# Kernel tuning notes

Hardware: AMD Instinct MI355X
Metric: run time of the kernel (lower is better)

## Reference

```python
import jax, jax.numpy as jnp
import numpy as np


def insert_tdl(tdl, x):
    # Shift delay line: newest sample at row 0, drop oldest row.
    return jnp.concatenate([x, tdl[:-1]], axis=0)


def setup_inputs() -> dict:
    key = jax.random.key(0)
    ks = jax.random.split(key, 17)
    B = 16384            # batch of parallel simulations (columns)
    H = 1024             # controller hidden size
    Hp = 1024            # plant hidden size
    Dci = Dcr = Dco = 64 # controller TDL depths
    Dpi = Dpo = 64       # plant TDL depths
    f = lambda k, s: jax.random.normal(k, s, dtype=jnp.float32)
    return {
        "reference": f(ks[0], (1, B)),
        "citdl": f(ks[1], (Dci, B)),
        "crtdl": f(ks[2], (Dcr, B)),
        "cotdl": f(ks[3], (Dco, B)),
        "pitdl": f(ks[4], (Dpi - 1, B)),  # fresh controller output a2 completes the line
        "potdl": f(ks[5], (Dpo, B)),
        # controller parameters (trainable in the original)
        "ciw": 0.01 * f(ks[6], (H, Dci)),
        "crw": 0.01 * f(ks[7], (H, Dcr)),
        "cow": 0.01 * f(ks[8], (H, Dco)),
        "cb1": 0.01 * f(ks[9], (H, 1)),
        "clw": 0.01 * f(ks[10], (1, H)),
        "cb2": 0.01 * f(ks[11], (1, 1)),
        # plant parameters (detached/frozen in the original)
        "piw": 0.01 * f(ks[12], (Hp, Dpi)),
        "p_ow": 0.01 * f(ks[13], (Hp, Dpo)),
        "pb1": 0.01 * f(ks[14], (Hp, 1)),
        "plw": 0.01 * f(ks[15], (1, Hp)),
        "pb2": 0.01 * f(ks[16], (1, 1)),
    }


def reference(reference, citdl, crtdl, cotdl, pitdl, potdl,
              ciw, crw, cow, cb1, clw, cb2,
              piw, p_ow, pb1, plw, pb2):
    # Controller MLP
    n1 = ciw @ citdl + crw @ crtdl + cow @ cotdl + cb1   # [H, B]
    a1 = jnp.tanh(n1)
    a2 = clw @ a1 + cb2                                   # [1, B] controller output
    # Plant MLP (frozen model of the plant)
    pdelay = jnp.concatenate([pitdl, a2], axis=0)         # [Dpi, B]
    n3 = piw @ pdelay + p_ow @ potdl + pb1                # [Hp, B]
    a3 = jnp.tanh(n3)
    a4 = plw @ a3 + pb2                                   # [1, B] plant output
    # TDL shift/insert updates
    citdl = insert_tdl(citdl, a2)
    crtdl = insert_tdl(crtdl, reference)
    cotdl = insert_tdl(cotdl, a4)
    pitdl = insert_tdl(pitdl, a2)
    potdl = insert_tdl(potdl, a4)
    return (a4, citdl, crtdl, cotdl, pitdl, potdl)
```

## Files before the change

### kernel.cpp

```cpp
#include <hip/hip_runtime.h>

#define B_COLS 16384
#define BT 64
#define NWAVES 8
#define NT 4
#define X1_STRIDE 200
#define X2_STRIDE 136

#define OFS_A4 0
#define OFS_CI 16384
#define OFS_CR 1064960
#define OFS_CO 2113536
#define OFS_PI 3162112
#define OFS_PO 4194304

typedef short bf16x8_t __attribute__((ext_vector_type(8)));
typedef float f32x4_t __attribute__((ext_vector_type(4)));

__device__ __forceinline__ unsigned short bftrunc(float f) {
    return (unsigned short)(__float_as_uint(f) >> 16);
}
__device__ __forceinline__ unsigned int pk2(float lo, float hi) {
    return __builtin_amdgcn_perm(__float_as_uint(hi), __float_as_uint(lo), 0x07060302u);
}
__device__ __forceinline__ float tanh_fast(float x) {
    x = fminf(1.5f, fmaxf(-1.5f, x));
    float x2 = x * x;
    float num = x * (15.0f + x2);
    float den = 15.0f + 6.0f * x2;
    return num * __builtin_amdgcn_rcpf(den);
}

extern "C" __global__ __launch_bounds__(512, 2)
void fused_cell(const float* __restrict__ ref,
                const float* __restrict__ citdl,
                const float* __restrict__ crtdl,
                const float* __restrict__ cotdl,
                const float* __restrict__ pitdl,
                const float* __restrict__ potdl,
                const float* __restrict__ ciw,
                const float* __restrict__ crw,
                const float* __restrict__ cow,
                const float* __restrict__ cb1,
                const float* __restrict__ clw,
                const float* __restrict__ cb2,
                const float* __restrict__ piw,
                const float* __restrict__ p_ow,
                const float* __restrict__ pb1,
                const float* __restrict__ plw,
                const float* __restrict__ pb2,
                float* __restrict__ out)
{
    __shared__ unsigned short X1T[BT * X1_STRIDE];
    __shared__ unsigned short X2T[BT * X2_STRIDE];
    __shared__ float redbuf[NWAVES * BT];

    const int tid  = threadIdx.x;
    const int wave = tid >> 6;
    const int lane = tid & 63;
    const int quad = lane >> 4;
    const int l15  = lane & 15;
    const int c0   = blockIdx.x * BT;

    {
        const int w8 = wave * 8;
        #pragma unroll
        for (int pass = 0; pass < 3; ++pass) {
            int k = pass * 64 + lane;
            const float* src; int d;
            if (k < 64)       { src = citdl; d = k; }
            else if (k < 128) { src = crtdl; d = k - 64; }
            else              { src = cotdl; d = k - 128; }
            const float* p = src + (size_t)d * B_COLS + c0 + w8;
            float4 v0 = *(const float4*)(p);
            float4 v1 = *(const float4*)(p + 4);
            unsigned short* dst = &X1T[w8 * X1_STRIDE + k];
            dst[0 * X1_STRIDE] = bftrunc(v0.x);
            dst[1 * X1_STRIDE] = bftrunc(v0.y);
            dst[2 * X1_STRIDE] = bftrunc(v0.z);
            dst[3 * X1_STRIDE] = bftrunc(v0.w);
            dst[4 * X1_STRIDE] = bftrunc(v1.x);
            dst[5 * X1_STRIDE] = bftrunc(v1.y);
            dst[6 * X1_STRIDE] = bftrunc(v1.z);
            dst[7 * X1_STRIDE] = bftrunc(v1.w);
        }
        #pragma unroll
        for (int pass = 0; pass < 2; ++pass) {
            int k = pass * 64 + lane;
            if (k != 63) {
                const float* src; int d;
                if (k < 63) { src = pitdl; d = k; }
                else        { src = potdl; d = k - 64; }
                const float* p = src + (size_t)d * B_COLS + c0 + w8;
                float4 v0 = *(const float4*)(p);
                float4 v1 = *(const float4*)(p + 4);
                unsigned short* dst = &X2T[w8 * X2_STRIDE + k];
                dst[0 * X2_STRIDE] = bftrunc(v0.x);
                dst[1 * X2_STRIDE] = bftrunc(v0.y);
                dst[2 * X2_STRIDE] = bftrunc(v0.z);
                dst[3 * X2_STRIDE] = bftrunc(v0.w);
                dst[4 * X2_STRIDE] = bftrunc(v1.x);
                dst[5 * X2_STRIDE] = bftrunc(v1.y);
                dst[6 * X2_STRIDE] = bftrunc(v1.z);
                dst[7 * X2_STRIDE] = bftrunc(v1.w);
            }
        }
    }
    __syncthreads();

    bf16x8_t B1[6][NT];
    #pragma unroll
    for (int kk = 0; kk < 6; ++kk)
        #pragma unroll
        for (int nt = 0; nt < NT; ++nt)
            B1[kk][nt] = *(const bf16x8_t*)&X1T[(nt * 16 + l15) * X1_STRIDE + kk * 32 + quad * 8];

    float sc[NT] = {0.f, 0.f, 0.f, 0.f};

    #pragma unroll
    for (int mt = 0; mt < 8; ++mt) {
        const int hbase  = wave * 128 + mt * 16;
        const int hrow_a = hbase + l15;
        f32x4_t acc[NT];
        #pragma unroll
        for (int nt = 0; nt < NT; ++nt) acc[nt] = (f32x4_t){0.f, 0.f, 0.f, 0.f};

        #pragma unroll
        for (int kk = 0; kk < 6; ++kk) {
            const float* wsrc = (kk < 2) ? ciw : (kk < 4) ? crw : cow;
            const int cofs = (kk & 1) * 32;
            const float* wp = wsrc + (size_t)hrow_a * 64 + cofs + quad * 8;
            float4 a0 = *(const float4*)(wp);
            float4 a1 = *(const float4*)(wp + 4);
            union { bf16x8_t v; unsigned int u[4]; } A;
            A.u[0] = pk2(a0.x, a0.y);
            A.u[1] = pk2(a0.z, a0.w);
            A.u[2] = pk2(a1.x, a1.y);
            A.u[3] = pk2(a1.z, a1.w);
            #pragma unroll
            for (int nt = 0; nt < NT; ++nt)
                acc[nt] = __builtin_amdgcn_mfma_f32_16x16x32_bf16(A.v, B1[kk][nt], acc[nt], 0, 0, 0);
        }
        const int hr = hbase + quad * 4;
        float4 cb = *(const float4*)(cb1 + hr);
        float4 cl = *(const float4*)(clw + hr);
        const float cbv[4] = {cb.x, cb.y, cb.z, cb.w};
        const float clv[4] = {cl.x, cl.y, cl.z, cl.w};
        #pragma unroll
        for (int r = 0; r < 4; ++r) {
            #pragma unroll
            for (int nt = 0; nt < NT; ++nt)
                sc[nt] += clv[r] * tanh_fast(acc[nt][r] + cbv[r]);
        }
    }

    #pragma unroll
    for (int nt = 0; nt < NT; ++nt) {
        sc[nt] += __shfl_xor(sc[nt], 16);
        sc[nt] += __shfl_xor(sc[nt], 32);
    }
    if (lane < 16) {
        #pragma unroll
        for (int nt = 0; nt < NT; ++nt)
            redbuf[wave * BT + nt * 16 + lane] = sc[nt];
    }
    __syncthreads();

    if (tid < BT) {
        float s = 0.f;
        #pragma unroll
        for (int w = 0; w < NWAVES; ++w) s += redbuf[w * BT + tid];
        s += cb2[0];
        X2T[tid * X2_STRIDE + 63] = bftrunc(s);
        out[OFS_CI + c0 + tid] = s;
        out[OFS_PI + c0 + tid] = s;
    }
    __syncthreads();

    bf16x8_t B2[4][NT];
    #pragma unroll
    for (int kk = 0; kk < 4; ++kk)
        #pragma unroll
        for (int nt = 0; nt < NT; ++nt)
            B2[kk][nt] = *(const bf16x8_t*)&X2T[(nt * 16 + l15) * X2_STRIDE + kk * 32 + quad * 8];

    float s4[NT] = {0.f, 0.f, 0.f, 0.f};

    #pragma unroll
    for (int mt = 0; mt < 8; ++mt) {
        const int hbase  = wave * 128 + mt * 16;
        const int hrow_a = hbase + l15;
        f32x4_t acc[NT];
        #pragma unroll
        for (int nt = 0; nt < NT; ++nt) acc[nt] = (f32x4_t){0.f, 0.f, 0.f, 0.f};

        #pragma unroll
        for (int kk = 0; kk < 4; ++kk) {
            const float* wsrc = (kk < 2) ? piw : p_ow;
            const int cofs = (kk & 1) * 32;
            const float* wp = wsrc + (size_t)hrow_a * 64 + cofs + quad * 8;
            float4 a0 = *(const float4*)(wp);
            float4 a1 = *(const float4*)(wp + 4);
            union { bf16x8_t v; unsigned int u[4]; } A;
            A.u[0] = pk2(a0.x, a0.y);
            A.u[1] = pk2(a0.z, a0.w);
            A.u[2] = pk2(a1.x, a1.y);
            A.u[3] = pk2(a1.z, a1.w);
            #pragma unroll
            for (int nt = 0; nt < NT; ++nt)
                acc[nt] = __builtin_amdgcn_mfma_f32_16x16x32_bf16(A.v, B2[kk][nt], acc[nt], 0, 0, 0);
        }
        const int hr = hbase + quad * 4;
        float4 pb = *(const float4*)(pb1 + hr);
        float4 pl = *(const float4*)(plw + hr);
        const float pbv[4] = {pb.x, pb.y, pb.z, pb.w};
        const float plv[4] = {pl.x, pl.y, pl.z, pl.w};
        #pragma unroll
        for (int r = 0; r < 4; ++r) {
            #pragma unroll
            for (int nt = 0; nt < NT; ++nt)
                s4[nt] += plv[r] * tanh_fast(acc[nt][r] + pbv[r]);
        }
    }

    #pragma unroll
    for (int nt = 0; nt < NT; ++nt) {
        s4[nt] += __shfl_xor(s4[nt], 16);
        s4[nt] += __shfl_xor(s4[nt], 32);
    }
    if (lane < 16) {
        #pragma unroll
        for (int nt = 0; nt < NT; ++nt)
            redbuf[wave * BT + nt * 16 + lane] = s4[nt];
    }
    __syncthreads();

    if (tid < BT) {
        float s = 0.f;
        #pragma unroll
        for (int w = 0; w < NWAVES; ++w) s += redbuf[w * BT + tid];
        s += pb2[0];
        out[OFS_A4 + c0 + tid] = s;
        out[OFS_CO + c0 + tid] = s;
        out[OFS_PO + c0 + tid] = s;
    }

    {
        const int colo = c0 + (tid & 15) * 4;
        const int r0   = tid >> 4;
        for (int d = r0; d < 63; d += 32) {
            float4 v = *(const float4*)(citdl + (size_t)d * B_COLS + colo);
            *(float4*)(out + OFS_CI + (size_t)(d + 1) * B_COLS + colo) = v;
        }
        for (int d = r0; d < 63; d += 32) {
            float4 v = *(const float4*)(crtdl + (size_t)d * B_COLS + colo);
            *(float4*)(out + OFS_CR + (size_t)(d + 1) * B_COLS + colo) = v;
        }
        for (int d = r0; d < 63; d += 32) {
            float4 v = *(const float4*)(cotdl + (size_t)d * B_COLS + colo);
            *(float4*)(out + OFS_CO + (size_t)(d + 1) * B_COLS + colo) = v;
        }
        for (int d = r0; d < 62; d += 32) {
            float4 v = *(const float4*)(pitdl + (size_t)d * B_COLS + colo);
            *(float4*)(out + OFS_PI + (size_t)(d + 1) * B_COLS + colo) = v;
        }
        for (int d = r0; d < 63; d += 32) {
            float4 v = *(const float4*)(potdl + (size_t)d * B_COLS + colo);
            *(float4*)(out + OFS_PO + (size_t)(d + 1) * B_COLS + colo) = v;
        }
        if (tid < 16) {
            float4 v = *(const float4*)(ref + c0 + tid * 4);
            *(float4*)(out + OFS_CR + c0 + tid * 4) = v;
        }
    }
}

extern "C" void kernel_launch(void* const* d_in, const int* in_sizes, int n_in,
                              void* d_out, int out_size, void* d_ws, size_t ws_size,
                              hipStream_t stream) {
    (void)in_sizes; (void)n_in; (void)out_size; (void)d_ws; (void)ws_size;
    fused_cell<<<256, 512, 0, stream>>>(
        (const float*)d_in[0],  (const float*)d_in[1],
        (const float*)d_in[2],  (const float*)d_in[3],
        (const float*)d_in[4],  (const float*)d_in[5],
        (const float*)d_in[6],  (const float*)d_in[7],
        (const float*)d_in[8],  (const float*)d_in[9],
        (const float*)d_in[10], (const float*)d_in[11],
        (const float*)d_in[12], (const float*)d_in[13],
        (const float*)d_in[14], (const float*)d_in[15],
        (const float*)d_in[16],
        (float*)d_out);
}
```

Measured before the change: 151.9 us.

## Split TDL shift copies into separate copy blocks and pre-convert weights to bf16

The delay-line shift copies move out of the 256 compute blocks into 2520 extra copy-only blocks that stream rows with float4 loads and stores, so the copy traffic can spread across all CUs instead of trailing each compute block. A small prep kernel also converts the five weight matrices to bf16 in the workspace once per call, halving weight load bytes and removing per-block packing. This adds a second kernel launch and a larger grid, and the bf16 path only runs when the workspace is big enough.

```diff
diff --git a/kernel.cpp b/kernel.cpp
--- a/kernel.cpp
+++ b/kernel.cpp
@@ -7,6 +7,10 @@
 #define X1_STRIDE 200
 #define X2_STRIDE 136
 
+#define NCOMPUTE 256
+#define NCOPY 2520
+#define COPY_TOTAL 1290240
+
 #define OFS_A4 0
 #define OFS_CI 16384
 #define OFS_CR 1064960
@@ -14,6 +18,13 @@
 #define OFS_PI 3162112
 #define OFS_PO 4194304
 
+#define W_CIW 0
+#define W_CRW 65536
+#define W_COW 131072
+#define W_PIW 196608
+#define W_POW 262144
+#define W_TOTAL 327680
+
 typedef short bf16x8_t __attribute__((ext_vector_type(8)));
 typedef float f32x4_t __attribute__((ext_vector_type(4)));
 
@@ -31,7 +42,29 @@
     return num * __builtin_amdgcn_rcpf(den);
 }
 
-extern "C" __global__ __launch_bounds__(512, 2)
+extern "C" __global__ __launch_bounds__(256)
+void prep_weights(const float* __restrict__ ciw, const float* __restrict__ crw,
+                  const float* __restrict__ cow, const float* __restrict__ piw,
+                  const float* __restrict__ p_ow, unsigned short* __restrict__ wbf)
+{
+    int idx8 = blockIdx.x * 256 + threadIdx.x;
+    const float* src;
+    int base = idx8 * 8;
+    if      (idx8 < 8192)  { src = ciw  + base; }
+    else if (idx8 < 16384) { src = crw  + base - W_CRW; }
+    else if (idx8 < 24576) { src = cow  + base - W_COW; }
+    else if (idx8 < 32768) { src = piw  + base - W_PIW; }
+    else                   { src = p_ow + base - W_POW; }
+    float4 a = *(const float4*)(src);
+    float4 b = *(const float4*)(src + 4);
+    uint4 o;
+    o.x = pk2(a.x, a.y); o.y = pk2(a.z, a.w);
+    o.z = pk2(b.x, b.y); o.w = pk2(b.z, b.w);
+    *(uint4*)(wbf + base) = o;
+}
+
+template<bool BF16W>
+__global__ __launch_bounds__(512, 2)
 void fused_cell(const float* __restrict__ ref,
                 const float* __restrict__ citdl,
                 const float* __restrict__ crtdl,
@@ -49,13 +82,32 @@
                 const float* __restrict__ pb1,
                 const float* __restrict__ plw,
                 const float* __restrict__ pb2,
+                const unsigned short* __restrict__ wbf,
                 float* __restrict__ out)
 {
     __shared__ unsigned short X1T[BT * X1_STRIDE];
     __shared__ unsigned short X2T[BT * X2_STRIDE];
     __shared__ float redbuf[NWAVES * BT];
 
-    const int tid  = threadIdx.x;
+    const int tid = threadIdx.x;
+
+    if (blockIdx.x >= NCOMPUTE) {
+        int idx = (blockIdx.x - NCOMPUTE) * 512 + tid;
+        for (; idx < COPY_TOTAL; idx += NCOPY * 512) {
+            int r  = idx >> 12;
+            int c4 = (idx & 4095) << 2;
+            const float* s; float* d;
+            if      (r < 63)  { s = citdl + (size_t)r         * B_COLS; d = out + OFS_CI + (size_t)(r + 1)   * B_COLS; }
+            else if (r < 126) { s = crtdl + (size_t)(r - 63)  * B_COLS; d = out + OFS_CR + (size_t)(r - 62)  * B_COLS; }
+            else if (r < 189) { s = cotdl + (size_t)(r - 126) * B_COLS; d = out + OFS_CO + (size_t)(r - 125) * B_COLS; }
+            else if (r < 251) { s = pitdl + (size_t)(r - 189) * B_COLS; d = out + OFS_PI + (size_t)(r - 188) * B_COLS; }
+            else if (r < 314) { s = potdl + (size_t)(r - 251) * B_COLS; d = out + OFS_PO + (size_t)(r - 250) * B_COLS; }
+            else              { s = ref;                                d = out + OFS_CR; }
+            *(float4*)(d + c4) = *(const float4*)(s + c4);
+        }
+        return;
+    }
+
     const int wave = tid >> 6;
     const int lane = tid & 63;
     const int quad = lane >> 4;
@@ -75,14 +127,10 @@
             float4 v0 = *(const float4*)(p);
             float4 v1 = *(const float4*)(p + 4);
             unsigned short* dst = &X1T[w8 * X1_STRIDE + k];
-            dst[0 * X1_STRIDE] = bftrunc(v0.x);
-            dst[1 * X1_STRIDE] = bftrunc(v0.y);
-            dst[2 * X1_STRIDE] = bftrunc(v0.z);
-            dst[3 * X1_STRIDE] = bftrunc(v0.w);
-            dst[4 * X1_STRIDE] = bftrunc(v1.x);
-            dst[5 * X1_STRIDE] = bftrunc(v1.y);
-            dst[6 * X1_STRIDE] = bftrunc(v1.z);
-            dst[7 * X1_STRIDE] = bftrunc(v1.w);
+            dst[0 * X1_STRIDE] = bftrunc(v0.x); dst[1 * X1_STRIDE] = bftrunc(v0.y);
+            dst[2 * X1_STRIDE] = bftrunc(v0.z); dst[3 * X1_STRIDE] = bftrunc(v0.w);
+            dst[4 * X1_STRIDE] = bftrunc(v1.x); dst[5 * X1_STRIDE] = bftrunc(v1.y);
+            dst[6 * X1_STRIDE] = bftrunc(v1.z); dst[7 * X1_STRIDE] = bftrunc(v1.w);
         }
         #pragma unroll
         for (int pass = 0; pass < 2; ++pass) {
@@ -95,14 +143,10 @@
                 float4 v0 = *(const float4*)(p);
                 float4 v1 = *(const float4*)(p + 4);
                 unsigned short* dst = &X2T[w8 * X2_STRIDE + k];
-                dst[0 * X2_STRIDE] = bftrunc(v0.x);
-                dst[1 * X2_STRIDE] = bftrunc(v0.y);
-                dst[2 * X2_STRIDE] = bftrunc(v0.z);
-                dst[3 * X2_STRIDE] = bftrunc(v0.w);
-                dst[4 * X2_STRIDE] = bftrunc(v1.x);
-                dst[5 * X2_STRIDE] = bftrunc(v1.y);
-                dst[6 * X2_STRIDE] = bftrunc(v1.z);
-                dst[7 * X2_STRIDE] = bftrunc(v1.w);
+                dst[0 * X2_STRIDE] = bftrunc(v0.x); dst[1 * X2_STRIDE] = bftrunc(v0.y);
+                dst[2 * X2_STRIDE] = bftrunc(v0.z); dst[3 * X2_STRIDE] = bftrunc(v0.w);
+                dst[4 * X2_STRIDE] = bftrunc(v1.x); dst[5 * X2_STRIDE] = bftrunc(v1.y);
+                dst[6 * X2_STRIDE] = bftrunc(v1.z); dst[7 * X2_STRIDE] = bftrunc(v1.w);
             }
         }
     }
@@ -127,16 +171,18 @@
 
         #pragma unroll
         for (int kk = 0; kk < 6; ++kk) {
-            const float* wsrc = (kk < 2) ? ciw : (kk < 4) ? crw : cow;
-            const int cofs = (kk & 1) * 32;
-            const float* wp = wsrc + (size_t)hrow_a * 64 + cofs + quad * 8;
-            float4 a0 = *(const float4*)(wp);
-            float4 a1 = *(const float4*)(wp + 4);
             union { bf16x8_t v; unsigned int u[4]; } A;
-            A.u[0] = pk2(a0.x, a0.y);
-            A.u[1] = pk2(a0.z, a0.w);
-            A.u[2] = pk2(a1.x, a1.y);
-            A.u[3] = pk2(a1.z, a1.w);
+            if (BF16W) {
+                const unsigned short* wsrc = wbf + ((kk < 2) ? W_CIW : (kk < 4) ? W_CRW : W_COW);
+                A.v = *(const bf16x8_t*)(wsrc + (size_t)hrow_a * 64 + (kk & 1) * 32 + quad * 8);
+            } else {
+                const float* wsrc = (kk < 2) ? ciw : (kk < 4) ? crw : cow;
+                const float* wp = wsrc + (size_t)hrow_a * 64 + (kk & 1) * 32 + quad * 8;
+                float4 a0 = *(const float4*)(wp);
+                float4 a1 = *(const float4*)(wp + 4);
+                A.u[0] = pk2(a0.x, a0.y); A.u[1] = pk2(a0.z, a0.w);
+                A.u[2] = pk2(a1.x, a1.y); A.u[3] = pk2(a1.z, a1.w);
+            }
             #pragma unroll
             for (int nt = 0; nt < NT; ++nt)
                 acc[nt] = __builtin_amdgcn_mfma_f32_16x16x32_bf16(A.v, B1[kk][nt], acc[nt], 0, 0, 0);
@@ -147,11 +193,10 @@
         const float cbv[4] = {cb.x, cb.y, cb.z, cb.w};
         const float clv[4] = {cl.x, cl.y, cl.z, cl.w};
         #pragma unroll
-        for (int r = 0; r < 4; ++r) {
+        for (int r = 0; r < 4; ++r)
             #pragma unroll
             for (int nt = 0; nt < NT; ++nt)
                 sc[nt] += clv[r] * tanh_fast(acc[nt][r] + cbv[r]);
-        }
     }
 
     #pragma unroll
@@ -159,11 +204,10 @@
         sc[nt] += __shfl_xor(sc[nt], 16);
         sc[nt] += __shfl_xor(sc[nt], 32);
     }
-    if (lane < 16) {
+    if (lane < 16)
         #pragma unroll
         for (int nt = 0; nt < NT; ++nt)
             redbuf[wave * BT + nt * 16 + lane] = sc[nt];
-    }
     __syncthreads();
 
     if (tid < BT) {
@@ -196,16 +240,18 @@
 
         #pragma unroll
         for (int kk = 0; kk < 4; ++kk) {
-            const float* wsrc = (kk < 2) ? piw : p_ow;
-            const int cofs = (kk & 1) * 32;
-            const float* wp = wsrc + (size_t)hrow_a * 64 + cofs + quad * 8;
-            float4 a0 = *(const float4*)(wp);
-            float4 a1 = *(const float4*)(wp + 4);
             union { bf16x8_t v; unsigned int u[4]; } A;
-            A.u[0] = pk2(a0.x, a0.y);
-            A.u[1] = pk2(a0.z, a0.w);
-            A.u[2] = pk2(a1.x, a1.y);
-            A.u[3] = pk2(a1.z, a1.w);
+            if (BF16W) {
+                const unsigned short* wsrc = wbf + ((kk < 2) ? W_PIW : W_POW);
+                A.v = *(const bf16x8_t*)(wsrc + (size_t)hrow_a * 64 + (kk & 1) * 32 + quad * 8);
+            } else {
+                const float* wsrc = (kk < 2) ? piw : p_ow;
+                const float* wp = wsrc + (size_t)hrow_a * 64 + (kk & 1) * 32 + quad * 8;
+                float4 a0 = *(const float4*)(wp);
+                float4 a1 = *(const float4*)(wp + 4);
+                A.u[0] = pk2(a0.x, a0.y); A.u[1] = pk2(a0.z, a0.w);
+                A.u[2] = pk2(a1.x, a1.y); A.u[3] = pk2(a1.z, a1.w);
+            }
             #pragma unroll
             for (int nt = 0; nt < NT; ++nt)
                 acc[nt] = __builtin_amdgcn_mfma_f32_16x16x32_bf16(A.v, B2[kk][nt], acc[nt], 0, 0, 0);
@@ -216,11 +262,10 @@
         const float pbv[4] = {pb.x, pb.y, pb.z, pb.w};
         const float plv[4] = {pl.x, pl.y, pl.z, pl.w};
         #pragma unroll
-        for (int r = 0; r < 4; ++r) {
+        for (int r = 0; r < 4; ++r)
             #pragma unroll
             for (int nt = 0; nt < NT; ++nt)
                 s4[nt] += plv[r] * tanh_fast(acc[nt][r] + pbv[r]);
-        }
     }
 
     #pragma unroll
@@ -228,11 +273,10 @@
         s4[nt] += __shfl_xor(s4[nt], 16);
         s4[nt] += __shfl_xor(s4[nt], 32);
     }
-    if (lane < 16) {
+    if (lane < 16)
         #pragma unroll
         for (int nt = 0; nt < NT; ++nt)
             redbuf[wave * BT + nt * 16 + lane] = s4[nt];
-    }
     __syncthreads();
 
     if (tid < BT) {
@@ -244,50 +288,42 @@
         out[OFS_CO + c0 + tid] = s;
         out[OFS_PO + c0 + tid] = s;
     }
-
-    {
-        const int colo = c0 + (tid & 15) * 4;
-        const int r0   = tid >> 4;
-        for (int d = r0; d < 63; d += 32) {
-            float4 v = *(const float4*)(citdl + (size_t)d * B_COLS + colo);
-            *(float4*)(out + OFS_CI + (size_t)(d + 1) * B_COLS + colo) = v;
-        }
-        for (int d = r0; d < 63; d += 32) {
-            float4 v = *(const float4*)(crtdl + (size_t)d * B_COLS + colo);
-            *(float4*)(out + OFS_CR + (size_t)(d + 1) * B_COLS + colo) = v;
-        }
-        for (int d = r0; d < 63; d += 32) {
-            float4 v = *(const float4*)(cotdl + (size_t)d * B_COLS + colo);
-            *(float4*)(out + OFS_CO + (size_t)(d + 1) * B_COLS + colo) = v;
-        }
-        for (int d = r0; d < 62; d += 32) {
-            float4 v = *(const float4*)(pitdl + (size_t)d * B_COLS + colo);
-            *(float4*)(out + OFS_PI + (size_t)(d + 1) * B_COLS + colo) = v;
-        }
-        for (int d = r0; d < 63; d += 32) {
-            float4 v = *(const float4*)(potdl + (size_t)d * B_COLS + colo);
-            *(float4*)(out + OFS_PO + (size_t)(d + 1) * B_COLS + colo) = v;
-        }
-        if (tid < 16) {
-            float4 v = *(const float4*)(ref + c0 + tid * 4);
-            *(float4*)(out + OFS_CR + c0 + tid * 4) = v;
-        }
-    }
 }
 
 extern "C" void kernel_launch(void* const* d_in, const int* in_sizes, int n_in,
                               void* d_out, int out_size, void* d_ws, size_t ws_size,
                               hipStream_t stream) {
-    (void)in_sizes; (void)n_in; (void)out_size; (void)d_ws; (void)ws_size;
-    fused_cell<<<256, 512, 0, stream>>>(
-        (const float*)d_in[0],  (const float*)d_in[1],
-        (const float*)d_in[2],  (const float*)d_in[3],
-        (const float*)d_in[4],  (const float*)d_in[5],
-        (const float*)d_in[6],  (const float*)d_in[7],
-        (const float*)d_in[8],  (const float*)d_in[9],
-        (const float*)d_in[10], (const float*)d_in[11],
-        (const float*)d_in[12], (const float*)d_in[13],
-        (const float*)d_in[14], (const float*)d_in[15],
-        (const float*)d_in[16],
-        (float*)d_out);
-}
+    (void)in_sizes; (void)n_in; (void)out_size;
+    const float* ref   = (const float*)d_in[0];
+    const float* citdl = (const float*)d_in[1];
+    const float* crtdl = (const float*)d_in[2];
+    const float* cotdl = (const float*)d_in[3];
+    const float* pitdl = (const float*)d_in[4];
+    const float* potdl = (const float*)d_in[5];
+    const float* ciw   = (const float*)d_in[6];
+    const float* crw   = (const float*)d_in[7];
+    const float* cow   = (const float*)d_in[8];
+    const float* cb1   = (const float*)d_in[9];
+    const float* clw   = (const float*)d_in[10];
+    const float* cb2   = (const float*)d_in[11];
+    const float* piw   = (const float*)d_in[12];
+    const float* p_ow  = (const float*)d_in[13];
+    const float* pb1   = (const float*)d_in[14];
+    const float* plw   = (const float*)d_in[15];
+    const float* pb2   = (const float*)d_in[16];
+    float* out = (float*)d_out;
+
+    if (ws_size >= (size_t)W_TOTAL * 2) {
+        unsigned short* wbf = (unsigned short*)d_ws;
+        prep_weights<<<160, 256, 0, stream>>>(ciw, crw, cow, piw, p_ow, wbf);
+        fused_cell<true><<<NCOMPUTE + NCOPY, 512, 0, stream>>>(
+            ref, citdl, crtdl, cotdl, pitdl, potdl,
+            ciw, crw, cow, cb1, clw, cb2, piw, p_ow, pb1, plw, pb2,
+            wbf, out);
+    } else {
+        fused_cell<false><<<NCOMPUTE + NCOPY, 512, 0, stream>>>(
+            ref, citdl, crtdl, cotdl, pitdl, potdl,
+            ciw, crw, cow, cb1, clw, cb2, piw, p_ow, pb1, plw, pb2,
+            nullptr, out);
+    }
+}
```

Result: faster. 133.0 us (-12.4%).
